# Kernel optimization log

Hardware: AMD Instinct MI355X
Metric: run time of the kernel (lower is better)

## Reference

```python
import jax, jax.numpy as jnp
import numpy as np

H = 128; D_T = 512; D_C = 256
NT = 20000; NC = 100000
E_TC = 100000; E_SIM = 800000; E_TS = 640000
K_APPNP = 10; ALPHA = 0.2


def setup_inputs() -> dict:
    key = jax.random.key(0)
    ki = iter(jax.random.split(key, 64))
    def nrm(shape, scale=1.0):
        return jax.random.normal(next(ki), shape, jnp.float32) * scale
    inp = {
        'table_x': nrm((NT, D_T)),
        'column_x': nrm((NC, D_C)),
        'q': nrm((D_T,)),
    }
    # layer-1 SAGEConv params per edge type: (src_dim, dst_dim)
    dims1 = {'tc': (D_T, D_C), 'rev': (D_C, D_T), 'cs': (D_C, D_C),
             'ns': (D_C, D_C), 'ds': (D_C, D_C), 'ts': (D_T, D_T)}
    for et, (dsrc, ddst) in dims1.items():
        inp['Wl1_' + et] = nrm((dsrc, H), 1.0 / np.sqrt(dsrc))
        inp['bl1_' + et] = jnp.zeros((H,), jnp.float32)
        inp['Wr1_' + et] = nrm((ddst, H), 1.0 / np.sqrt(ddst))
    # layer-2: only the convs that feed the 'table' output are needed
    for et in ('rev', 'ts'):
        inp['Wl2_' + et] = nrm((H, H), 1.0 / np.sqrt(H))
        inp['bl2_' + et] = jnp.zeros((H,), jnp.float32)
        inp['Wr2_' + et] = nrm((H, H), 1.0 / np.sqrt(H))
    inp['Wq'] = nrm((D_T, H), 1.0 / np.sqrt(D_T))
    inp['bq'] = jnp.zeros((H,), jnp.float32)
    inp['Wlin'] = nrm((H, 1), 1.0 / np.sqrt(H))
    inp['blin'] = jnp.zeros((1,), jnp.float32)
    inp['ts_ew'] = jax.random.uniform(next(ki), (E_TS,), jnp.float32)
    inp['tc_src'] = jax.random.randint(next(ki), (E_TC,), 0, NT)
    inp['tc_dst'] = jax.random.randint(next(ki), (E_TC,), 0, NC)
    inp['cs_ei'] = jax.random.randint(next(ki), (2, E_SIM), 0, NC)
    inp['ns_ei'] = jax.random.randint(next(ki), (2, E_SIM), 0, NC)
    inp['ds_ei'] = jax.random.randint(next(ki), (2, E_SIM), 0, NC)
    inp['ts_ei'] = jax.random.randint(next(ki), (2, E_TS), 0, NT)
    return inp


def _sage(xs, xd, src, dst, Wl, bl, Wr, n_dst):
    # PyG SAGEConv: lin_l(mean_{j in N(i)} x_j) + lin_r(x_i).
    # Linear commutes with mean, so project src features first (cheap gather).
    m = (xs @ Wl)[src]                                     # [E, H]
    s = jax.ops.segment_sum(m, dst, num_segments=n_dst)    # [n_dst, H]
    c = jax.ops.segment_sum(jnp.ones(src.shape, m.dtype), dst, num_segments=n_dst)
    return s / jnp.maximum(c, 1.0)[:, None] + bl + xd @ Wr


def _appnp(x, src, dst, ew, n):
    # gcn_norm with self-loops (fill value 1), then K personalized-PageRank steps
    loop = jnp.arange(n)
    s2 = jnp.concatenate([src, loop])
    d2 = jnp.concatenate([dst, loop])
    w2 = jnp.concatenate([ew, jnp.ones((n,), x.dtype)])
    deg = jax.ops.segment_sum(w2, d2, num_segments=n)
    dis = jnp.where(deg > 0, 1.0 / jnp.sqrt(deg), 0.0)
    norm = dis[s2] * w2 * dis[d2]                           # [E+n]
    def step(z, _):
        h = jax.ops.segment_sum(norm[:, None] * z[s2], d2, num_segments=n)
        return (1.0 - ALPHA) * h + ALPHA * x, None
    z, _ = jax.lax.scan(step, x, None, length=K_APPNP)
    return z


def reference(table_x, column_x, q, Wl1_tc, bl1_tc, Wr1_tc, Wl1_rev, bl1_rev, Wr1_rev,
              Wl1_cs, bl1_cs, Wr1_cs, Wl1_ns, bl1_ns, Wr1_ns, Wl1_ds, bl1_ds, Wr1_ds,
              Wl1_ts, bl1_ts, Wr1_ts, Wl2_rev, bl2_rev, Wr2_rev, Wl2_ts, bl2_ts, Wr2_ts,
              Wq, bq, Wlin, blin, ts_ew, tc_src, tc_dst, cs_ei, ns_ei, ds_ei, ts_ei):
    nT, nC = table_x.shape[0], column_x.shape[0]
    # ---- HeteroConv layer 1 (sum over edge types per destination type) ----
    col1 = (_sage(table_x, column_x, tc_src, tc_dst, Wl1_tc, bl1_tc, Wr1_tc, nC)
            + _sage(column_x, column_x, cs_ei[0], cs_ei[1], Wl1_cs, bl1_cs, Wr1_cs, nC)
            + _sage(column_x, column_x, ns_ei[0], ns_ei[1], Wl1_ns, bl1_ns, Wr1_ns, nC)
            + _sage(column_x, column_x, ds_ei[0], ds_ei[1], Wl1_ds, bl1_ds, Wr1_ds, nC))
    tab1 = (_sage(column_x, table_x, tc_dst, tc_src, Wl1_rev, bl1_rev, Wr1_rev, nT)
            + _sage(table_x, table_x, ts_ei[0], ts_ei[1], Wl1_ts, bl1_ts, Wr1_ts, nT))
    col1 = jax.nn.relu(col1)
    tab1 = jax.nn.relu(tab1)
    # ---- HeteroConv layer 2 (only the 'table' output is consumed) ----
    tab2 = (_sage(col1, tab1, tc_dst, tc_src, Wl2_rev, bl2_rev, Wr2_rev, nT)
            + _sage(tab1, tab1, ts_ei[0], ts_ei[1], Wl2_ts, bl2_ts, Wr2_ts, nT))
    # ---- retrieval-weighted query injection ----
    qv = q @ Wq + bq                                        # [H]
    eps = 1e-12
    xr = table_x / jnp.maximum(jnp.linalg.norm(table_x, axis=1, keepdims=True), eps)
    qr = q / jnp.maximum(jnp.linalg.norm(q), eps)
    wgt = jnp.maximum(xr @ qr, 0.0)                         # [nT]
    z0 = wgt[:, None] * qv[None, :]                         # [nT, H]
    # ---- APPNP diffusion over the table-sim graph ----
    z = _appnp(tab2 + z0, ts_ei[0], ts_ei[1], ts_ew, nT)
    return (z @ Wlin + blin)[:, 0]
```

## Files before the change

kernel.cpp:

```cpp
#include <hip/hip_runtime.h>

#define NT 20000
#define NC 100000
#define DT 512
#define DC 256
#define E_TC 100000
#define E_SIM 800000
#define E_TS 640000

#define KB_COL 0
#define KB_TAB (4 * NC)
#define NKEY   (4 * NC + 2 * NT)
#define NED_AB (3 * E_SIM + E_TC + E_TC + E_TS)
#define COLSTR 112
#define TABSTR 96
#define GCOL 782
#define GTAB 313
#define NFILL 365
#define GRID_MEGA (GCOL + GTAB + NFILL)

typedef float f32x4 __attribute__((ext_vector_type(4)));
typedef __bf16 bf16x8 __attribute__((ext_vector_type(8)));


struct WD { const float* w0; const float* w1; const float* w2; const float* w3;
            __bf16* out; int K; int kshift; int ebase; };
struct WD8 { WD d[8]; };

__global__ void wprep_all(WD8 ds, int total) {
    int i = blockIdx.x * blockDim.x + threadIdx.x;
    if (i >= total) return;
#pragma unroll
    for (int s = 7; s >= 0; --s) {
        if (i >= ds.d[s].ebase) {
            const WD d = ds.d[s];
            const int idx = i - d.ebase;
            const int n = idx >> d.kshift;
            const int k = idx & (d.K - 1);
            float v = d.w0[(size_t)k * 128 + n];
            if (d.w1) v += d.w1[(size_t)k * 128 + n];
            if (d.w2) v += d.w2[(size_t)k * 128 + n];
            if (d.w3) v += d.w3[(size_t)k * 128 + n];
            d.out[(size_t)n * d.K + k] = (__bf16)v;
            return;
        }
    }
}

__global__ void vecprep(const float* __restrict__ q, const float* __restrict__ Wq,
                        const float* __restrict__ bq,
                        const float* __restrict__ Wr2_rev, const float* __restrict__ Wr2_ts,
                        const float* __restrict__ Wl2_rev, const float* __restrict__ Wl2_ts,
                        const float* __restrict__ bl2_rev, const float* __restrict__ bl2_ts,
                        const float* __restrict__ Wlin,
                        const float* __restrict__ bl1_tc, const float* __restrict__ bl1_cs,
                        const float* __restrict__ bl1_ns, const float* __restrict__ bl1_ds,
                        const float* __restrict__ bl1_rev, const float* __restrict__ bl1_ts,
                        float* __restrict__ biasC, float* __restrict__ biasT1,
                        float* __restrict__ w2s, float* __restrict__ wrev,
                        float* __restrict__ wts, float* __restrict__ sc) {
    const int t = threadIdx.x;
    biasC[t] = bl1_tc[t] + bl1_cs[t] + bl1_ns[t] + bl1_ds[t];
    biasT1[t] = bl1_rev[t] + bl1_ts[t];
    float a = 0.f, b = 0.f, c = 0.f;
    for (int h = 0; h < 128; ++h) {
        const float wl = Wlin[h];
        a = fmaf(Wr2_rev[(size_t)t * 128 + h] + Wr2_ts[(size_t)t * 128 + h], wl, a);
        b = fmaf(Wl2_rev[(size_t)t * 128 + h], wl, b);
        c = fmaf(Wl2_ts[(size_t)t * 128 + h], wl, c);
    }
    w2s[t] = a; wrev[t] = b; wts[t] = c;
    float qv = bq[t];
    for (int k = 0; k < 512; ++k) qv = fmaf(q[k], Wq[(size_t)k * 128 + t], qv);
    __shared__ float sh[128];
    sh[t] = qv * Wlin[t];
    __syncthreads();
    for (int st = 64; st >= 1; st >>= 1) { if (t < st) sh[t] += sh[t + st]; __syncthreads(); }
    if (t == 0) sc[0] = sh[0];
    __syncthreads();
    sh[t] = (bl2_rev[t] + bl2_ts[t]) * Wlin[t];
    __syncthreads();
    for (int st = 64; st >= 1; st >>= 1) { if (t < st) sh[t] += sh[t + st]; __syncthreads(); }
    if (t == 0) sc[1] = sh[0];
    __syncthreads();
    float ss = 0.f;
    for (int k = t; k < 512; k += 128) { const float v = q[k]; ss = fmaf(v, v, ss); }
    sh[t] = ss;
    __syncthreads();
    for (int st = 64; st >= 1; st >>= 1) { if (t < st) sh[t] += sh[t + st]; __syncthreads(); }
    if (t == 0) sc[2] = fmaxf(sqrtf(sh[0]), 1e-12f);
}


struct B5 { const __bf16* p[5]; };
struct Y5 { __bf16* p[5]; };
struct B3 { const __bf16* p[3]; };
struct Y3 { __bf16* p[3]; };
struct ED { const int* dst; const int* src; int E; int ebase; int ng; int g;
            int keybase; int srcoff; int ts; };
struct ED6 { ED d[6]; };

__launch_bounds__(256, 2)
__global__ void mega(const float* __restrict__ Xc, B5 wpc, const float* __restrict__ biasC,
                     Y5 ypc, const float* __restrict__ Xt, B3 wpt,
                     const float* __restrict__ biasT, Y3 ypt,
                     const float* __restrict__ q, const float* __restrict__ sc,
                     float* __restrict__ wgt, ED6 cds, const float* __restrict__ ew_ts,
                     float* __restrict__ deg, int* __restrict__ cur,
                     int* __restrict__ ed_idx, int2* __restrict__ edT) {
    __shared__ __bf16 Bs[128 * 256];
    const int bb = blockIdx.x;
    const int bt = bb & 3;
    const int t = threadIdx.x;

    if (bt == 3) {
        for (int e = (bb >> 2) * 256 + t; e < NED_AB; e += NFILL * 256) {
#pragma unroll
            for (int i = 5; i >= 0; --i) {
                if (e >= cds.d[i].ebase) {
                    const ED d = cds.d[i];
                    const int le = e - d.ebase;
                    const int dstv = d.dst[le];
                    const int key = d.keybase + dstv * d.ng + d.g;
                    const int srcv = d.src[le];
                    const int slot = atomicAdd(&cur[key], 1);
                    if (key < KB_TAB) {
                        const int g = key & 3;
                        const int cap = (g < 3) ? 32 : 16;
                        if (slot < cap)
                            ed_idx[(key >> 2) * COLSTR + g * 32 + slot] = d.srcoff + srcv;
                    } else {
                        const int k2 = key - KB_TAB;
                        if (k2 & 1) {
                            const float ew = ew_ts[le];
                            atomicAdd(&deg[dstv], ew);
                            if (slot < 72)
                                edT[(k2 >> 1) * TABSTR + 24 + slot] =
                                    make_int2(NC + srcv, __float_as_int(ew));
                        } else {
                            if (slot < 24)
                                edT[(k2 >> 1) * TABSTR + slot] = make_int2(srcv, 0);
                        }
                    }
                    break;
                }
            }
        }
        return;
    }

    const int gi = (bb >> 2) * 3 + bt;
    const int lane = t & 63;
    const int wave = t >> 6;
    const int l15 = lane & 15;
    const int kg = lane >> 4;

    if (gi < GCOL) {
        const int rowbase = gi * 128 + wave * 32;
        bf16x8 af[2][8];
#pragma unroll
        for (int m = 0; m < 2; ++m) {
            int r = rowbase + m * 16 + l15;
            r = (r < NC) ? r : (NC - 1);
            const float* baseA = Xc + (size_t)r * 256 + kg * 8;
#pragma unroll
            for (int ks = 0; ks < 8; ++ks) {
                const float4 x0 = *reinterpret_cast<const float4*>(baseA + ks * 32);
                const float4 x1 = *reinterpret_cast<const float4*>(baseA + ks * 32 + 4);
                bf16x8 tt;
                tt[0] = (__bf16)x0.x; tt[1] = (__bf16)x0.y; tt[2] = (__bf16)x0.z; tt[3] = (__bf16)x0.w;
                tt[4] = (__bf16)x1.x; tt[5] = (__bf16)x1.y; tt[6] = (__bf16)x1.z; tt[7] = (__bf16)x1.w;
                af[m][ks] = tt;
            }
        }
#pragma unroll
        for (int o = 0; o < 5; ++o) {
            __syncthreads();
            const __bf16* Wt = wpc.p[o];
#pragma unroll
            for (int i = 0; i < 16; ++i) {
                const int u = t + i * 256;
                const int row = u >> 5;
                const int ku = u & 31;
                const bf16x8 v = *reinterpret_cast<const bf16x8*>(Wt + (size_t)row * 256 + ku * 8);
                *reinterpret_cast<bf16x8*>(&Bs[row * 256 + ((ku ^ (row & 7)) << 3)]) = v;
            }
            __syncthreads();
            f32x4 acc[2][8];
#pragma unroll
            for (int m = 0; m < 2; ++m)
#pragma unroll
                for (int n = 0; n < 8; ++n) acc[m][n] = (f32x4)0.f;
#pragma unroll
            for (int ks = 0; ks < 8; ++ks) {
                const int ku = ks * 4 + kg;
#pragma unroll
                for (int n = 0; n < 8; ++n) {
                    const int r = n * 16 + l15;
                    const bf16x8 bf = *reinterpret_cast<const bf16x8*>(&Bs[r * 256 + ((ku ^ (r & 7)) << 3)]);
                    acc[0][n] = __builtin_amdgcn_mfma_f32_16x16x32_bf16(af[0][ks], bf, acc[0][n], 0, 0, 0);
                    acc[1][n] = __builtin_amdgcn_mfma_f32_16x16x32_bf16(af[1][ks], bf, acc[1][n], 0, 0, 0);
                }
            }
            __bf16* Y = ypc.p[o];
#pragma unroll
            for (int n = 0; n < 8; ++n) {
                const int col = n * 16 + l15;
                const float bv = (o == 0) ? biasC[col] : 0.f;
#pragma unroll
                for (int m = 0; m < 2; ++m)
#pragma unroll
                    for (int rr = 0; rr < 4; ++rr) {
                        const int row = rowbase + m * 16 + kg * 4 + rr;
                        if (row < NC) Y[(size_t)row * 128 + col] = (__bf16)(acc[m][n][rr] + bv);
                    }
            }
        }
        return;
    }

    {
        const int gb = gi - GCOL;
        const int rowbase = gb * 64 + wave * 16;
        const int r0 = rowbase + l15;
        const bool rv = r0 < NT;
        const int rc = rv ? r0 : (NT - 1);
        const float* baseA = Xt + (size_t)rc * 512 + kg * 8;

        bf16x8 af[16];
        float dot = 0.f, ss = 0.f;
#pragma unroll
        for (int ks = 0; ks < 16; ++ks) {
            const float4 x0 = *reinterpret_cast<const float4*>(baseA + ks * 32);
            const float4 x1 = *reinterpret_cast<const float4*>(baseA + ks * 32 + 4);
            const float4 q0 = *reinterpret_cast<const float4*>(q + kg * 8 + ks * 32);
            const float4 q1 = *reinterpret_cast<const float4*>(q + kg * 8 + ks * 32 + 4);
            dot += x0.x * q0.x + x0.y * q0.y + x0.z * q0.z + x0.w * q0.w
                 + x1.x * q1.x + x1.y * q1.y + x1.z * q1.z + x1.w * q1.w;
            ss += x0.x * x0.x + x0.y * x0.y + x0.z * x0.z + x0.w * x0.w
                + x1.x * x1.x + x1.y * x1.y + x1.z * x1.z + x1.w * x1.w;
            bf16x8 tt;
            tt[0] = (__bf16)x0.x; tt[1] = (__bf16)x0.y; tt[2] = (__bf16)x0.z; tt[3] = (__bf16)x0.w;
            tt[4] = (__bf16)x1.x; tt[5] = (__bf16)x1.y; tt[6] = (__bf16)x1.z; tt[7] = (__bf16)x1.w;
            af[ks] = tt;
        }
        dot += __shfl_xor(dot, 16); dot += __shfl_xor(dot, 32);
        ss  += __shfl_xor(ss, 16);  ss  += __shfl_xor(ss, 32);
        if (lane < 16 && rv) {
            const float nx = fmaxf(sqrtf(ss), 1e-12f);
            wgt[r0] = fmaxf(dot, 0.f) / (nx * sc[2]);
        }
#pragma unroll
        for (int o = 0; o < 3; ++o) {
            f32x4 acc[8];
#pragma unroll
            for (int n = 0; n < 8; ++n) acc[n] = (f32x4)0.f;
            const __bf16* Wt = wpt.p[o];
#pragma unroll
            for (int c = 0; c < 2; ++c) {
                __syncthreads();
#pragma unroll
                for (int i = 0; i < 16; ++i) {
                    const int u = t + i * 256;
                    const int row = u >> 5;
                    const int ku = u & 31;
                    const bf16x8 v = *reinterpret_cast<const bf16x8*>(Wt + (size_t)row * 512 + c * 256 + ku * 8);
                    *reinterpret_cast<bf16x8*>(&Bs[row * 256 + ((ku ^ (row & 7)) << 3)]) = v;
                }
                __syncthreads();
#pragma unroll
                for (int ks = 0; ks < 8; ++ks) {
                    const int ku = ks * 4 + kg;
#pragma unroll
                    for (int n = 0; n < 8; ++n) {
                        const int r = n * 16 + l15;
                        const bf16x8 bf = *reinterpret_cast<const bf16x8*>(&Bs[r * 256 + ((ku ^ (r & 7)) << 3)]);
                        acc[n] = __builtin_amdgcn_mfma_f32_16x16x32_bf16(af[c * 8 + ks], bf, acc[n], 0, 0, 0);
                    }
                }
            }
            __bf16* Y = ypt.p[o];
#pragma unroll
            for (int n = 0; n < 8; ++n) {
                const int col = n * 16 + l15;
                const float bv = (o == 0) ? biasT[col] : 0.f;
#pragma unroll
                for (int rr = 0; rr < 4; ++rr) {
                    const int row = rowbase + kg * 4 + rr;
                    if (row < NT) Y[(size_t)row * 128 + col] = (__bf16)(acc[n][rr] + bv);
                }
            }
        }
    }
}


__global__ void deg_to_dis(float* __restrict__ deg, int n) {
    int i = blockIdx.x * blockDim.x + threadIdx.x;
    if (i < n) {
        float d = deg[i];
        deg[i] = (d > 0.f) ? (1.0f / sqrtf(d)) : 0.f;
    }
}

__global__ void fill_f32(float* __restrict__ p, float v, int n) {
    int i = blockIdx.x * blockDim.x + threadIdx.x;
    if (i < n) p[i] = v;
}

__global__ void nrm_pass(int2* __restrict__ edT, const int* __restrict__ cur,
                         const float* __restrict__ dis) {
    int i = blockIdx.x * blockDim.x + threadIdx.x;
    if (i >= NT * 72) return;
    const int row = i / 72;
    const int s = i - row * 72;
    int lg = cur[KB_TAB + row * 2 + 1];
    lg = (lg < 72) ? lg : 72;
    if (s >= lg) return;
    const int2 v = edT[row * TABSTR + 24 + s];
    const float nv = dis[v.x - NC] * __int_as_float(v.y) * dis[row];
    edT[row * TABSTR + 24 + s].y = __float_as_int(nv);
}


__launch_bounds__(256)
__global__ void col_fused(const __bf16* __restrict__ selfRow, const __bf16* __restrict__ featCat,
                          const int* __restrict__ cur, const int* __restrict__ ed_idx,
                          const float* __restrict__ wvec, float* __restrict__ outv, int n) {
    const int wave = threadIdx.x >> 6;
    const int lane = threadIdx.x & 63;
    const int sg = lane >> 4;
    const int sl = lane & 15;
    const int row = blockIdx.x * 4 + wave;
    if (row >= n) return;
    const int4 l4 = *reinterpret_cast<const int4*>(&cur[row * 4]);
    int len[4];
    len[0] = (l4.x < 32) ? l4.x : 32;
    len[1] = (l4.y < 32) ? l4.y : 32;
    len[2] = (l4.z < 32) ? l4.z : 32;
    len[3] = (l4.w < 16) ? l4.w : 16;
    const int rowbase = row * COLSTR;
    float s8[8] = {0.f, 0.f, 0.f, 0.f, 0.f, 0.f, 0.f, 0.f};
#pragma unroll
    for (int g = 0; g < 4; ++g) {
        const int lg = len[g];
        if (lg <= 0) continue;
        const int base = rowbase + g * 32;
        const float w = 1.0f / (float)lg;
        int j = sg;
        for (; j + 4 < lg; j += 8) {
            const int s0 = ed_idx[base + j];
            const int s1 = ed_idx[base + j + 4];
            const bf16x8 v0 = *reinterpret_cast<const bf16x8*>(&featCat[(size_t)s0 * 128 + sl * 8]);
            const bf16x8 v1 = *reinterpret_cast<const bf16x8*>(&featCat[(size_t)s1 * 128 + sl * 8]);
#pragma unroll
            for (int t = 0; t < 8; ++t) {
                s8[t] = fmaf(w, (float)v0[t], s8[t]);
                s8[t] = fmaf(w, (float)v1[t], s8[t]);
            }
        }
        if (j < lg) {
            const int s0 = ed_idx[base + j];
            const bf16x8 v0 = *reinterpret_cast<const bf16x8*>(&featCat[(size_t)s0 * 128 + sl * 8]);
#pragma unroll
            for (int t = 0; t < 8; ++t) s8[t] = fmaf(w, (float)v0[t], s8[t]);
        }
    }
#pragma unroll
    for (int t = 0; t < 8; ++t) {
        s8[t] += __shfl_xor(s8[t], 16);
        s8[t] += __shfl_xor(s8[t], 32);
    }
    const bf16x8 gv = *reinterpret_cast<const bf16x8*>(&selfRow[(size_t)row * 128 + sl * 8]);
    const float4 w0 = *reinterpret_cast<const float4*>(&wvec[sl * 8]);
    const float4 w1 = *reinterpret_cast<const float4*>(&wvec[sl * 8 + 4]);
    const float ww[8] = {w0.x, w0.y, w0.z, w0.w, w1.x, w1.y, w1.z, w1.w};
    float d = 0.f;
#pragma unroll
    for (int t = 0; t < 8; ++t) d = fmaf(fmaxf(s8[t] + (float)gv[t], 0.f), ww[t], d);
#pragma unroll
    for (int off = 8; off; off >>= 1) d += __shfl_xor(d, off);
    if (lane == 0) outv[row] = d;
}

__launch_bounds__(256)
__global__ void tab_fused(const __bf16* __restrict__ selfRow, const __bf16* __restrict__ featCat,
                          const int* __restrict__ cur, const int2* __restrict__ edT,
                          const float* __restrict__ wa, const float* __restrict__ wb,
                          float* __restrict__ ya, float* __restrict__ yb, int n) {
    const int wave = threadIdx.x >> 6;
    const int lane = threadIdx.x & 63;
    const int sg = lane >> 4;
    const int sl = lane & 15;
    const int row = blockIdx.x * 4 + wave;
    if (row >= n) return;
    const int2 l2 = *reinterpret_cast<const int2*>(&cur[KB_TAB + row * 2]);
    int len[2];
    len[0] = (l2.x < 24) ? l2.x : 24;
    len[1] = (l2.y < 72) ? l2.y : 72;
    const int rowbase = row * TABSTR;
    float s8[8] = {0.f, 0.f, 0.f, 0.f, 0.f, 0.f, 0.f, 0.f};
#pragma unroll
    for (int g = 0; g < 2; ++g) {
        const int lg = len[g];
        if (lg <= 0) continue;
        const int base = rowbase + g * 24;
        const float w = 1.0f / (float)lg;
        int j = sg;
        for (; j + 4 < lg; j += 8) {
            const int s0 = edT[base + j].x;
            const int s1 = edT[base + j + 4].x;
            const bf16x8 v0 = *reinterpret_cast<const bf16x8*>(&featCat[(size_t)s0 * 128 + sl * 8]);
            const bf16x8 v1 = *reinterpret_cast<const bf16x8*>(&featCat[(size_t)s1 * 128 + sl * 8]);
#pragma unroll
            for (int t = 0; t < 8; ++t) {
                s8[t] = fmaf(w, (float)v0[t], s8[t]);
                s8[t] = fmaf(w, (float)v1[t], s8[t]);
            }
        }
        if (j < lg) {
            const int s0 = edT[base + j].x;
            const bf16x8 v0 = *reinterpret_cast<const bf16x8*>(&featCat[(size_t)s0 * 128 + sl * 8]);
#pragma unroll
            for (int t = 0; t < 8; ++t) s8[t] = fmaf(w, (float)v0[t], s8[t]);
        }
    }
#pragma unroll
    for (int t = 0; t < 8; ++t) {
        s8[t] += __shfl_xor(s8[t], 16);
        s8[t] += __shfl_xor(s8[t], 32);
    }
    const bf16x8 gv = *reinterpret_cast<const bf16x8*>(&selfRow[(size_t)row * 128 + sl * 8]);
    const float4 a0 = *reinterpret_cast<const float4*>(&wa[sl * 8]);
    const float4 a1 = *reinterpret_cast<const float4*>(&wa[sl * 8 + 4]);
    const float4 b0 = *reinterpret_cast<const float4*>(&wb[sl * 8]);
    const float4 b1 = *reinterpret_cast<const float4*>(&wb[sl * 8 + 4]);
    const float wwa[8] = {a0.x, a0.y, a0.z, a0.w, a1.x, a1.y, a1.z, a1.w};
    const float wwb[8] = {b0.x, b0.y, b0.z, b0.w, b1.x, b1.y, b1.z, b1.w};
    float da = 0.f, db = 0.f;
#pragma unroll
    for (int t = 0; t < 8; ++t) {
        const float rv = fmaxf(s8[t] + (float)gv[t], 0.f);
        da = fmaf(rv, wwa[t], da);
        db = fmaf(rv, wwb[t], db);
    }
#pragma unroll
    for (int off = 8; off; off >>= 1) { da += __shfl_xor(da, off); db += __shfl_xor(db, off); }
    if (lane == 0) { ya[row] = da; yb[row] = db; }
}


__launch_bounds__(256)
__global__ void y0_joint(const float* __restrict__ tvs, const float* __restrict__ val2,
                         const int* __restrict__ cur, const int2* __restrict__ edT,
                         const float* __restrict__ wgt, const float* __restrict__ sc,
                         float* __restrict__ y0, int n) {
    const int row = blockIdx.x * 16 + (threadIdx.x >> 4);
    const int l = threadIdx.x & 15;
    if (row >= n) return;
    const int2 l2 = *reinterpret_cast<const int2*>(&cur[KB_TAB + row * 2]);
    int len[2];
    len[0] = (l2.x < 24) ? l2.x : 24;
    len[1] = (l2.y < 72) ? l2.y : 72;
    const int rowbase = row * TABSTR;
    float s = 0.f;
#pragma unroll
    for (int g = 0; g < 2; ++g) {
        const int lg = len[g];
        if (lg <= 0) continue;
        const int base = rowbase + g * 24;
        const float w = 1.0f / (float)lg;
        for (int j = l; j < lg; j += 16) {
            int idx = edT[base + j].x;
            if (g == 1) idx -= NC;
            s = fmaf(w, val2[g == 1 ? (NC + idx) : idx], s);
        }
    }
#pragma unroll
    for (int off = 8; off; off >>= 1) s += __shfl_xor(s, off);
    if (l == 0) y0[row] = tvs[row] + sc[1] + wgt[row] * sc[0] + s;
}

__launch_bounds__(256)
__global__ void appnp_s(const float* __restrict__ z, const float* __restrict__ y0,
                        const int* __restrict__ cur, const int2* __restrict__ edT,
                        const float* __restrict__ dis, float* __restrict__ zo,
                        const float* __restrict__ blin, float* __restrict__ out,
                        int n, int last) {
    const int row = blockIdx.x * 16 + (threadIdx.x >> 4);
    const int l = threadIdx.x & 15;
    if (row >= n) return;
    int lg = cur[KB_TAB + row * 2 + 1];
    lg = (lg < 72) ? lg : 72;
    const int base = row * TABSTR + 24;
    float s = 0.f;
    int j = l;
    for (; j + 16 < lg; j += 32) {
        const int2 p0 = edT[base + j];
        const int2 p1 = edT[base + j + 16];
        s = fmaf(__int_as_float(p0.y), z[p0.x - NC], s);
        s = fmaf(__int_as_float(p1.y), z[p1.x - NC], s);
    }
    if (j < lg) {
        const int2 p0 = edT[base + j];
        s = fmaf(__int_as_float(p0.y), z[p0.x - NC], s);
    }
#pragma unroll
    for (int off = 8; off; off >>= 1) s += __shfl_xor(s, off);
    if (l == 0) {
        const float d = dis[row];
        const float v = 0.8f * (s + d * d * z[row]) + 0.2f * y0[row];
        if (last) out[row] = v + blin[0];
        else zo[row] = v;
    }
}


extern "C" void kernel_launch(void* const* d_in, const int* in_sizes, int n_in,
                              void* d_out, int out_size, void* d_ws, size_t ws_size,
                              hipStream_t stream) {
    const float* table_x  = (const float*)d_in[0];
    const float* column_x = (const float*)d_in[1];
    const float* q        = (const float*)d_in[2];
    const float* Wl1_tc  = (const float*)d_in[3];  const float* bl1_tc  = (const float*)d_in[4];  const float* Wr1_tc  = (const float*)d_in[5];
    const float* Wl1_rev = (const float*)d_in[6];  const float* bl1_rev = (const float*)d_in[7];  const float* Wr1_rev = (const float*)d_in[8];
    const float* Wl1_cs  = (const float*)d_in[9];  const float* bl1_cs  = (const float*)d_in[10]; const float* Wr1_cs  = (const float*)d_in[11];
    const float* Wl1_ns  = (const float*)d_in[12]; const float* bl1_ns  = (const float*)d_in[13]; const float* Wr1_ns  = (const float*)d_in[14];
    const float* Wl1_ds  = (const float*)d_in[15]; const float* bl1_ds  = (const float*)d_in[16]; const float* Wr1_ds  = (const float*)d_in[17];
    const float* Wl1_ts  = (const float*)d_in[18]; const float* bl1_ts  = (const float*)d_in[19]; const float* Wr1_ts  = (const float*)d_in[20];
    const float* Wl2_rev = (const float*)d_in[21]; const float* bl2_rev = (const float*)d_in[22]; const float* Wr2_rev = (const float*)d_in[23];
    const float* Wl2_ts  = (const float*)d_in[24]; const float* bl2_ts  = (const float*)d_in[25]; const float* Wr2_ts  = (const float*)d_in[26];
    const float* Wq   = (const float*)d_in[27]; const float* bq   = (const float*)d_in[28];
    const float* Wlin = (const float*)d_in[29]; const float* blin = (const float*)d_in[30];
    const float* ts_ew = (const float*)d_in[31];
    const int* tc_src = (const int*)d_in[32];
    const int* tc_dst = (const int*)d_in[33];
    const int* cs_ei  = (const int*)d_in[34];
    const int* ns_ei  = (const int*)d_in[35];
    const int* ds_ei  = (const int*)d_in[36];
    const int* ts_ei  = (const int*)d_in[37];

    char* w = (char*)d_ws;
    size_t off = 0;
    auto alloc = [&](size_t bytes) -> void* {
        void* p = w + off;
        off += (bytes + 255) & ~(size_t)255;
        return p;
    };
    __bf16* featC = (__bf16*)alloc(((size_t)3 * NC + NT) * 128 * 2);
    __bf16* featT = (__bf16*)alloc(((size_t)NC + NT) * 128 * 2);
    __bf16* projC_cs  = featC;
    __bf16* projC_ns  = featC + (size_t)NC * 128;
    __bf16* projC_ds  = featC + (size_t)2 * NC * 128;
    __bf16* projT_tc  = featC + (size_t)3 * NC * 128;
    __bf16* projC_rev = featT;
    __bf16* projT_ts  = featT + (size_t)NC * 128;
    __bf16* gemmC = (__bf16*)alloc((size_t)NC * 128 * 2);
    __bf16* gemmT = (__bf16*)alloc((size_t)NT * 128 * 2);
    float* val2  = (float*)alloc((size_t)(NC + NT) * 4);
    float* f_colv = val2;
    float* f_tvt  = val2 + NC;
    float* f_tvs = (float*)alloc((size_t)NT * 4);
    float* f_wgt = (float*)alloc((size_t)NT * 4);
    float* f_dis = (float*)alloc((size_t)NT * 4);
    float* f_y0  = (float*)alloc((size_t)NT * 4);
    float* f_za  = (float*)alloc((size_t)NT * 4);
    float* f_zb  = (float*)alloc((size_t)NT * 4);
    __bf16* WtS1c  = (__bf16*)alloc((size_t)128 * 256 * 2);
    __bf16* Wt_cs  = (__bf16*)alloc((size_t)128 * 256 * 2);
    __bf16* Wt_ns  = (__bf16*)alloc((size_t)128 * 256 * 2);
    __bf16* Wt_ds  = (__bf16*)alloc((size_t)128 * 256 * 2);
    __bf16* Wt_rev = (__bf16*)alloc((size_t)128 * 256 * 2);
    __bf16* Wt_tc  = (__bf16*)alloc((size_t)128 * 512 * 2);
    __bf16* WtS1t  = (__bf16*)alloc((size_t)128 * 512 * 2);
    __bf16* Wt_ts  = (__bf16*)alloc((size_t)128 * 512 * 2);
    float* f_biasC  = (float*)alloc(128 * 4);
    float* f_biasT1 = (float*)alloc(128 * 4);
    float* f_w2s  = (float*)alloc(128 * 4);
    float* f_wrev = (float*)alloc(128 * 4);
    float* f_wts  = (float*)alloc(128 * 4);
    float* f_sc   = (float*)alloc(16 * 4);
    int* i_cur  = (int*)alloc((size_t)NKEY * 4);
    int* ed_idx = (int*)alloc((size_t)NC * COLSTR * 4);
    int2* edT   = (int2*)alloc((size_t)NT * TABSTR * 8);
    if (off > ws_size) return;

    auto cdiv = [](int a, int b) { return (a + b - 1) / b; };

    {
        WD8 ds;
        int eb = 0;
        auto set = [&](int i, const float* a, const float* b2, const float* c, const float* d2,
                       __bf16* o, int K, int ksh) {
            ds.d[i] = {a, b2, c, d2, o, K, ksh, eb};
            eb += 128 * K;
        };
        set(0, Wr1_tc, Wr1_cs, Wr1_ns, Wr1_ds, WtS1c, 256, 8);
        set(1, Wl1_cs, nullptr, nullptr, nullptr, Wt_cs, 256, 8);
        set(2, Wl1_ns, nullptr, nullptr, nullptr, Wt_ns, 256, 8);
        set(3, Wl1_ds, nullptr, nullptr, nullptr, Wt_ds, 256, 8);
        set(4, Wl1_rev, nullptr, nullptr, nullptr, Wt_rev, 256, 8);
        set(5, Wl1_tc, nullptr, nullptr, nullptr, Wt_tc, 512, 9);
        set(6, Wr1_rev, Wr1_ts, nullptr, nullptr, WtS1t, 512, 9);
        set(7, Wl1_ts, nullptr, nullptr, nullptr, Wt_ts, 512, 9);
        wprep_all<<<cdiv(eb, 256), 256, 0, stream>>>(ds, eb);
    }
    vecprep<<<1, 128, 0, stream>>>(q, Wq, bq, Wr2_rev, Wr2_ts, Wl2_rev, Wl2_ts,
                                   bl2_rev, bl2_ts, Wlin, bl1_tc, bl1_cs, bl1_ns, bl1_ds,
                                   bl1_rev, bl1_ts, f_biasC, f_biasT1,
                                   f_w2s, f_wrev, f_wts, f_sc);

    fill_f32<<<cdiv(NT, 256), 256, 0, stream>>>(f_dis, 1.0f, NT);
    hipMemsetAsync(i_cur, 0, (size_t)NKEY * 4, stream);

    ED6 cds;
    cds.d[0] = {cs_ei + E_SIM, cs_ei, E_SIM, 0,                  4, 0, KB_COL, 0,      0};
    cds.d[1] = {ns_ei + E_SIM, ns_ei, E_SIM, E_SIM,              4, 1, KB_COL, NC,     0};
    cds.d[2] = {ds_ei + E_SIM, ds_ei, E_SIM, 2 * E_SIM,          4, 2, KB_COL, 2 * NC, 0};
    cds.d[3] = {tc_dst, tc_src, E_TC, 3 * E_SIM,                 4, 3, KB_COL, 3 * NC, 0};
    cds.d[4] = {tc_src, tc_dst, E_TC, 3 * E_SIM + E_TC,          2, 0, KB_TAB, 0,      0};
    cds.d[5] = {ts_ei + E_TS, ts_ei, E_TS, 3 * E_SIM + 2 * E_TC, 2, 1, KB_TAB, NC,     1};

    {
        B5 wpc; wpc.p[0] = WtS1c; wpc.p[1] = Wt_cs; wpc.p[2] = Wt_ns; wpc.p[3] = Wt_ds; wpc.p[4] = Wt_rev;
        Y5 ypc; ypc.p[0] = gemmC; ypc.p[1] = projC_cs; ypc.p[2] = projC_ns; ypc.p[3] = projC_ds; ypc.p[4] = projC_rev;
        B3 wpt; wpt.p[0] = WtS1t; wpt.p[1] = Wt_tc; wpt.p[2] = Wt_ts;
        Y3 ypt; ypt.p[0] = gemmT; ypt.p[1] = projT_tc; ypt.p[2] = projT_ts;
        mega<<<GRID_MEGA, 256, 0, stream>>>(column_x, wpc, f_biasC, ypc,
                                            table_x, wpt, f_biasT1, ypt,
                                            q, f_sc, f_wgt, cds, ts_ew,
                                            f_dis, i_cur, ed_idx, edT);
    }

    deg_to_dis<<<cdiv(NT, 256), 256, 0, stream>>>(f_dis, NT);
    nrm_pass<<<cdiv(NT * 72, 256), 256, 0, stream>>>(edT, i_cur, f_dis);

    col_fused<<<cdiv(NC, 4), 256, 0, stream>>>(gemmC, featC, i_cur, ed_idx,
                                               f_wrev, f_colv, NC);
    tab_fused<<<cdiv(NT, 4), 256, 0, stream>>>(gemmT, featT, i_cur, edT,
                                               f_w2s, f_wts, f_tvs, f_tvt, NT);

    y0_joint<<<cdiv(NT, 16), 256, 0, stream>>>(f_tvs, val2, i_cur, edT,
                                               f_wgt, f_sc, f_y0, NT);

    const float* zin = f_y0;
    float* zout = f_za;
    for (int it = 0; it < 10; ++it) {
        const int last = (it == 9);
        appnp_s<<<cdiv(NT, 16), 256, 0, stream>>>(zin, f_y0, i_cur, edT,
                                                  f_dis, zout, blin, (float*)d_out, NT, last);
        zin = zout;
        zout = (zout == f_za) ? f_zb : f_za;
    }
}
```

Measured before the change: 579.5 us.

## Fold edge-bucket fill into extra waves inside each GEMM block of mega kernel

Drops the separate fill-only blocks from the fused projection/edge-bucketing kernel. Each GEMM block now gets two extra waves (384 threads) that do the atomic edge bucketing in chunks between the GEMM barriers, so the fill work runs alongside the MFMA work inside the same workgroup. It also simplifies the index arithmetic in y0_joint's gather. The intent is better overlap of latency-bound atomics with compute, at the cost of higher register and occupancy pressure from launch_bounds(384,3) and fill progress being tied to the GEMM barrier cadence.

```diff
diff --git a/kernel.cpp b/kernel.cpp
--- a/kernel.cpp
+++ b/kernel.cpp
@@ -16,8 +16,8 @@
 #define TABSTR 96
 #define GCOL 782
 #define GTAB 313
-#define NFILL 365
-#define GRID_MEGA (GCOL + GTAB + NFILL)
+#define GRID_MEGA (GCOL + GTAB)
+#define FILL_LANES (GRID_MEGA * 128)
 
 typedef float f32x4 __attribute__((ext_vector_type(4)));
 typedef __bf16 bf16x8 __attribute__((ext_vector_type(8)));
@@ -100,127 +100,141 @@
             int keybase; int srcoff; int ts; };
 struct ED6 { ED d[6]; };
 
-__launch_bounds__(256, 2)
-__global__ void mega(const float* __restrict__ Xc, B5 wpc, const float* __restrict__ biasC,
-                     Y5 ypc, const float* __restrict__ Xt, B3 wpt,
-                     const float* __restrict__ biasT, Y3 ypt,
-                     const float* __restrict__ q, const float* __restrict__ sc,
-                     float* __restrict__ wgt, ED6 cds, const float* __restrict__ ew_ts,
-                     float* __restrict__ deg, int* __restrict__ cur,
-                     int* __restrict__ ed_idx, int2* __restrict__ edT) {
+__launch_bounds__(384, 3)
+__global__ void mega2(const float* __restrict__ Xc, B5 wpc, const float* __restrict__ biasC,
+                      Y5 ypc, const float* __restrict__ Xt, B3 wpt,
+                      const float* __restrict__ biasT, Y3 ypt,
+                      const float* __restrict__ q, const float* __restrict__ sc,
+                      float* __restrict__ wgt, ED6 cds, const float* __restrict__ ew_ts,
+                      float* __restrict__ deg, int* __restrict__ cur,
+                      int* __restrict__ ed_idx, int2* __restrict__ edT) {
     __shared__ __bf16 Bs[128 * 256];
     const int bb = blockIdx.x;
-    const int bt = bb & 3;
     const int t = threadIdx.x;
-
-    if (bt == 3) {
-        for (int e = (bb >> 2) * 256 + t; e < NED_AB; e += NFILL * 256) {
-#pragma unroll
-            for (int i = 5; i >= 0; --i) {
-                if (e >= cds.d[i].ebase) {
-                    const ED d = cds.d[i];
-                    const int le = e - d.ebase;
-                    const int dstv = d.dst[le];
-                    const int key = d.keybase + dstv * d.ng + d.g;
-                    const int srcv = d.src[le];
-                    const int slot = atomicAdd(&cur[key], 1);
-                    if (key < KB_TAB) {
-                        const int g = key & 3;
-                        const int cap = (g < 3) ? 32 : 16;
-                        if (slot < cap)
-                            ed_idx[(key >> 2) * COLSTR + g * 32 + slot] = d.srcoff + srcv;
+    const bool fillw = (t >= 256);
+    int fe = bb * 128 + (t - 256);
+
+    auto fill_edge = [&](int e) {
+#pragma unroll
+        for (int i = 5; i >= 0; --i) {
+            if (e >= cds.d[i].ebase) {
+                const ED d = cds.d[i];
+                const int le = e - d.ebase;
+                const int dstv = d.dst[le];
+                const int key = d.keybase + dstv * d.ng + d.g;
+                const int srcv = d.src[le];
+                const int slot = atomicAdd(&cur[key], 1);
+                if (key < KB_TAB) {
+                    const int g = key & 3;
+                    const int cap = (g < 3) ? 32 : 16;
+                    if (slot < cap)
+                        ed_idx[(key >> 2) * COLSTR + g * 32 + slot] = d.srcoff + srcv;
+                } else {
+                    const int k2 = key - KB_TAB;
+                    if (k2 & 1) {
+                        const float ew = ew_ts[le];
+                        atomicAdd(&deg[dstv], ew);
+                        if (slot < 72)
+                            edT[(k2 >> 1) * TABSTR + 24 + slot] =
+                                make_int2(NC + srcv, __float_as_int(ew));
                     } else {
-                        const int k2 = key - KB_TAB;
-                        if (k2 & 1) {
-                            const float ew = ew_ts[le];
-                            atomicAdd(&deg[dstv], ew);
-                            if (slot < 72)
-                                edT[(k2 >> 1) * TABSTR + 24 + slot] =
-                                    make_int2(NC + srcv, __float_as_int(ew));
-                        } else {
-                            if (slot < 24)
-                                edT[(k2 >> 1) * TABSTR + slot] = make_int2(srcv, 0);
-                        }
+                        if (slot < 24)
+                            edT[(k2 >> 1) * TABSTR + slot] = make_int2(srcv, 0);
                     }
-                    break;
-                }
-            }
-        }
-        return;
-    }
-
-    const int gi = (bb >> 2) * 3 + bt;
+                }
+                return;
+            }
+        }
+    };
+    auto fill_chunk = [&](int n) {
+        for (int it = 0; it < n && fe < NED_AB; ++it) {
+            fill_edge(fe);
+            fe += FILL_LANES;
+        }
+    };
+
     const int lane = t & 63;
     const int wave = t >> 6;
     const int l15 = lane & 15;
     const int kg = lane >> 4;
 
-    if (gi < GCOL) {
-        const int rowbase = gi * 128 + wave * 32;
+    if (bb < GCOL) {
+        const int rowbase = bb * 128 + wave * 32;
         bf16x8 af[2][8];
-#pragma unroll
-        for (int m = 0; m < 2; ++m) {
-            int r = rowbase + m * 16 + l15;
-            r = (r < NC) ? r : (NC - 1);
-            const float* baseA = Xc + (size_t)r * 256 + kg * 8;
-#pragma unroll
-            for (int ks = 0; ks < 8; ++ks) {
-                const float4 x0 = *reinterpret_cast<const float4*>(baseA + ks * 32);
-                const float4 x1 = *reinterpret_cast<const float4*>(baseA + ks * 32 + 4);
-                bf16x8 tt;
-                tt[0] = (__bf16)x0.x; tt[1] = (__bf16)x0.y; tt[2] = (__bf16)x0.z; tt[3] = (__bf16)x0.w;
-                tt[4] = (__bf16)x1.x; tt[5] = (__bf16)x1.y; tt[6] = (__bf16)x1.z; tt[7] = (__bf16)x1.w;
-                af[m][ks] = tt;
+        if (!fillw) {
+#pragma unroll
+            for (int m = 0; m < 2; ++m) {
+                int r = rowbase + m * 16 + l15;
+                r = (r < NC) ? r : (NC - 1);
+                const float* baseA = Xc + (size_t)r * 256 + kg * 8;
+#pragma unroll
+                for (int ks = 0; ks < 8; ++ks) {
+                    const float4 x0 = *reinterpret_cast<const float4*>(baseA + ks * 32);
+                    const float4 x1 = *reinterpret_cast<const float4*>(baseA + ks * 32 + 4);
+                    bf16x8 tt;
+                    tt[0] = (__bf16)x0.x; tt[1] = (__bf16)x0.y; tt[2] = (__bf16)x0.z; tt[3] = (__bf16)x0.w;
+                    tt[4] = (__bf16)x1.x; tt[5] = (__bf16)x1.y; tt[6] = (__bf16)x1.z; tt[7] = (__bf16)x1.w;
+                    af[m][ks] = tt;
+                }
             }
         }
 #pragma unroll
         for (int o = 0; o < 5; ++o) {
             __syncthreads();
-            const __bf16* Wt = wpc.p[o];
-#pragma unroll
-            for (int i = 0; i < 16; ++i) {
-                const int u = t + i * 256;
-                const int row = u >> 5;
-                const int ku = u & 31;
-                const bf16x8 v = *reinterpret_cast<const bf16x8*>(Wt + (size_t)row * 256 + ku * 8);
-                *reinterpret_cast<bf16x8*>(&Bs[row * 256 + ((ku ^ (row & 7)) << 3)]) = v;
+            if (!fillw) {
+                const __bf16* Wt = wpc.p[o];
+#pragma unroll
+                for (int i = 0; i < 16; ++i) {
+                    const int u = t + i * 256;
+                    const int row = u >> 5;
+                    const int ku = u & 31;
+                    const bf16x8 v = *reinterpret_cast<const bf16x8*>(Wt + (size_t)row * 256 + ku * 8);
+                    *reinterpret_cast<bf16x8*>(&Bs[row * 256 + ((ku ^ (row & 7)) << 3)]) = v;
+                }
             }
             __syncthreads();
-            f32x4 acc[2][8];
-#pragma unroll
-            for (int m = 0; m < 2; ++m)
-#pragma unroll
-                for (int n = 0; n < 8; ++n) acc[m][n] = (f32x4)0.f;
-#pragma unroll
-            for (int ks = 0; ks < 8; ++ks) {
-                const int ku = ks * 4 + kg;
+            if (!fillw) {
+                f32x4 acc[2][8];
+#pragma unroll
+                for (int m = 0; m < 2; ++m)
+#pragma unroll
+                    for (int n = 0; n < 8; ++n) acc[m][n] = (f32x4)0.f;
+#pragma unroll
+                for (int ks = 0; ks < 8; ++ks) {
+                    const int ku = ks * 4 + kg;
+#pragma unroll
+                    for (int n = 0; n < 8; ++n) {
+                        const int r = n * 16 + l15;
+                        const bf16x8 bf = *reinterpret_cast<const bf16x8*>(&Bs[r * 256 + ((ku ^ (r & 7)) << 3)]);
+                        acc[0][n] = __builtin_amdgcn_mfma_f32_16x16x32_bf16(af[0][ks], bf, acc[0][n], 0, 0, 0);
+                        acc[1][n] = __builtin_amdgcn_mfma_f32_16x16x32_bf16(af[1][ks], bf, acc[1][n], 0, 0, 0);
+                    }
+                }
+                __bf16* Y = ypc.p[o];
 #pragma unroll
                 for (int n = 0; n < 8; ++n) {
-                    const int r = n * 16 + l15;
-                    const bf16x8 bf = *reinterpret_cast<const bf16x8*>(&Bs[r * 256 + ((ku ^ (r & 7)) << 3)]);
-                    acc[0][n] = __builtin_amdgcn_mfma_f32_16x16x32_bf16(af[0][ks], bf, acc[0][n], 0, 0, 0);
-                    acc[1][n] = __builtin_amdgcn_mfma_f32_16x16x32_bf16(af[1][ks], bf, acc[1][n], 0, 0, 0);
-                }
-            }
-            __bf16* Y = ypc.p[o];
-#pragma unroll
-            for (int n = 0; n < 8; ++n) {
-                const int col = n * 16 + l15;
-                const float bv = (o == 0) ? biasC[col] : 0.f;
-#pragma unroll
-                for (int m = 0; m < 2; ++m)
-#pragma unroll
-                    for (int rr = 0; rr < 4; ++rr) {
-                        const int row = rowbase + m * 16 + kg * 4 + rr;
-                        if (row < NC) Y[(size_t)row * 128 + col] = (__bf16)(acc[m][n][rr] + bv);
-                    }
-            }
+                    const int col = n * 16 + l15;
+                    const float bv = (o == 0) ? biasC[col] : 0.f;
+#pragma unroll
+                    for (int m = 0; m < 2; ++m)
+#pragma unroll
+                        for (int rr = 0; rr < 4; ++rr) {
+                            const int row = rowbase + m * 16 + kg * 4 + rr;
+                            if (row < NC) Y[(size_t)row * 128 + col] = (__bf16)(acc[m][n][rr] + bv);
+                        }
+                }
+            } else {
+                fill_chunk(5);
+            }
+        }
+        if (fillw) {
+            while (fe < NED_AB) { fill_edge(fe); fe += FILL_LANES; }
         }
         return;
     }
 
     {
-        const int gb = gi - GCOL;
+        const int gb = bb - GCOL;
         const int rowbase = gb * 64 + wave * 16;
         const int r0 = rowbase + l15;
         const bool rv = r0 < NT;
@@ -228,27 +242,29 @@
         const float* baseA = Xt + (size_t)rc * 512 + kg * 8;
 
         bf16x8 af[16];
-        float dot = 0.f, ss = 0.f;
-#pragma unroll
-        for (int ks = 0; ks < 16; ++ks) {
-            const float4 x0 = *reinterpret_cast<const float4*>(baseA + ks * 32);
-            const float4 x1 = *reinterpret_cast<const float4*>(baseA + ks * 32 + 4);
-            const float4 q0 = *reinterpret_cast<const float4*>(q + kg * 8 + ks * 32);
-            const float4 q1 = *reinterpret_cast<const float4*>(q + kg * 8 + ks * 32 + 4);
-            dot += x0.x * q0.x + x0.y * q0.y + x0.z * q0.z + x0.w * q0.w
-                 + x1.x * q1.x + x1.y * q1.y + x1.z * q1.z + x1.w * q1.w;
-            ss += x0.x * x0.x + x0.y * x0.y + x0.z * x0.z + x0.w * x0.w
-                + x1.x * x1.x + x1.y * x1.y + x1.z * x1.z + x1.w * x1.w;
-            bf16x8 tt;
-            tt[0] = (__bf16)x0.x; tt[1] = (__bf16)x0.y; tt[2] = (__bf16)x0.z; tt[3] = (__bf16)x0.w;
-            tt[4] = (__bf16)x1.x; tt[5] = (__bf16)x1.y; tt[6] = (__bf16)x1.z; tt[7] = (__bf16)x1.w;
-            af[ks] = tt;
-        }
-        dot += __shfl_xor(dot, 16); dot += __shfl_xor(dot, 32);
-        ss  += __shfl_xor(ss, 16);  ss  += __shfl_xor(ss, 32);
-        if (lane < 16 && rv) {
-            const float nx = fmaxf(sqrtf(ss), 1e-12f);
-            wgt[r0] = fmaxf(dot, 0.f) / (nx * sc[2]);
+        if (!fillw) {
+            float dot = 0.f, ss = 0.f;
+#pragma unroll
+            for (int ks = 0; ks < 16; ++ks) {
+                const float4 x0 = *reinterpret_cast<const float4*>(baseA + ks * 32);
+                const float4 x1 = *reinterpret_cast<const float4*>(baseA + ks * 32 + 4);
+                const float4 q0 = *reinterpret_cast<const float4*>(q + kg * 8 + ks * 32);
+                const float4 q1 = *reinterpret_cast<const float4*>(q + kg * 8 + ks * 32 + 4);
+                dot += x0.x * q0.x + x0.y * q0.y + x0.z * q0.z + x0.w * q0.w
+                     + x1.x * q1.x + x1.y * q1.y + x1.z * q1.z + x1.w * q1.w;
+                ss += x0.x * x0.x + x0.y * x0.y + x0.z * x0.z + x0.w * x0.w
+                    + x1.x * x1.x + x1.y * x1.y + x1.z * x1.z + x1.w * x1.w;
+                bf16x8 tt;
+                tt[0] = (__bf16)x0.x; tt[1] = (__bf16)x0.y; tt[2] = (__bf16)x0.z; tt[3] = (__bf16)x0.w;
+                tt[4] = (__bf16)x1.x; tt[5] = (__bf16)x1.y; tt[6] = (__bf16)x1.z; tt[7] = (__bf16)x1.w;
+                af[ks] = tt;
+            }
+            dot += __shfl_xor(dot, 16); dot += __shfl_xor(dot, 32);
+            ss  += __shfl_xor(ss, 16);  ss  += __shfl_xor(ss, 32);
+            if (lane < 16 && rv) {
+                const float nx = fmaxf(sqrtf(ss), 1e-12f);
+                wgt[r0] = fmaxf(dot, 0.f) / (nx * sc[2]);
+            }
         }
 #pragma unroll
         for (int o = 0; o < 3; ++o) {
@@ -259,37 +275,48 @@
 #pragma unroll
             for (int c = 0; c < 2; ++c) {
                 __syncthreads();
-#pragma unroll
-                for (int i = 0; i < 16; ++i) {
-                    const int u = t + i * 256;
-                    const int row = u >> 5;
-                    const int ku = u & 31;
-                    const bf16x8 v = *reinterpret_cast<const bf16x8*>(Wt + (size_t)row * 512 + c * 256 + ku * 8);
-                    *reinterpret_cast<bf16x8*>(&Bs[row * 256 + ((ku ^ (row & 7)) << 3)]) = v;
+                if (!fillw) {
+#pragma unroll
+                    for (int i = 0; i < 16; ++i) {
+                        const int u = t + i * 256;
+                        const int row = u >> 5;
+                        const int ku = u & 31;
+                        const bf16x8 v = *reinterpret_cast<const bf16x8*>(Wt + (size_t)row * 512 + c * 256 + ku * 8);
+                        *reinterpret_cast<bf16x8*>(&Bs[row * 256 + ((ku ^ (row & 7)) << 3)]) = v;
+                    }
                 }
                 __syncthreads();
-#pragma unroll
-                for (int ks = 0; ks < 8; ++ks) {
-                    const int ku = ks * 4 + kg;
-#pragma unroll
-                    for (int n = 0; n < 8; ++n) {
-                        const int r = n * 16 + l15;
-                        const bf16x8 bf = *reinterpret_cast<const bf16x8*>(&Bs[r * 256 + ((ku ^ (r & 7)) << 3)]);
-                        acc[n] = __builtin_amdgcn_mfma_f32_16x16x32_bf16(af[c * 8 + ks], bf, acc[n], 0, 0, 0);
+                if (!fillw) {
+#pragma unroll
+                    for (int ks = 0; ks < 8; ++ks) {
+                        const int ku = ks * 4 + kg;
+#pragma unroll
+                        for (int n = 0; n < 8; ++n) {
+                            const int r = n * 16 + l15;
+                            const bf16x8 bf = *reinterpret_cast<const bf16x8*>(&Bs[r * 256 + ((ku ^ (r & 7)) << 3)]);
+                            acc[n] = __builtin_amdgcn_mfma_f32_16x16x32_bf16(af[c * 8 + ks], bf, acc[n], 0, 0, 0);
+                        }
                     }
-                }
-            }
-            __bf16* Y = ypt.p[o];
-#pragma unroll
-            for (int n = 0; n < 8; ++n) {
-                const int col = n * 16 + l15;
-                const float bv = (o == 0) ? biasT[col] : 0.f;
-#pragma unroll
-                for (int rr = 0; rr < 4; ++rr) {
-                    const int row = rowbase + kg * 4 + rr;
-                    if (row < NT) Y[(size_t)row * 128 + col] = (__bf16)(acc[n][rr] + bv);
-                }
-            }
+                } else {
+                    fill_chunk(4);
+                }
+            }
+            if (!fillw) {
+                __bf16* Y = ypt.p[o];
+#pragma unroll
+                for (int n = 0; n < 8; ++n) {
+                    const int col = n * 16 + l15;
+                    const float bv = (o == 0) ? biasT[col] : 0.f;
+#pragma unroll
+                    for (int rr = 0; rr < 4; ++rr) {
+                        const int row = rowbase + kg * 4 + rr;
+                        if (row < NT) Y[(size_t)row * 128 + col] = (__bf16)(acc[n][rr] + bv);
+                    }
+                }
+            }
+        }
+        if (fillw) {
+            while (fe < NED_AB) { fill_edge(fe); fe += FILL_LANES; }
         }
     }
 }
@@ -471,9 +498,8 @@
         const int base = rowbase + g * 24;
         const float w = 1.0f / (float)lg;
         for (int j = l; j < lg; j += 16) {
-            int idx = edT[base + j].x;
-            if (g == 1) idx -= NC;
-            s = fmaf(w, val2[g == 1 ? (NC + idx) : idx], s);
+            const int idx = edT[base + j].x;
+            s = fmaf(w, val2[idx], s);
         }
     }
 #pragma unroll
@@ -626,10 +652,10 @@
         Y5 ypc; ypc.p[0] = gemmC; ypc.p[1] = projC_cs; ypc.p[2] = projC_ns; ypc.p[3] = projC_ds; ypc.p[4] = projC_rev;
         B3 wpt; wpt.p[0] = WtS1t; wpt.p[1] = Wt_tc; wpt.p[2] = Wt_ts;
         Y3 ypt; ypt.p[0] = gemmT; ypt.p[1] = projT_tc; ypt.p[2] = projT_ts;
-        mega<<<GRID_MEGA, 256, 0, stream>>>(column_x, wpc, f_biasC, ypc,
-                                            table_x, wpt, f_biasT1, ypt,
-                                            q, f_sc, f_wgt, cds, ts_ew,
-                                            f_dis, i_cur, ed_idx, edT);
+        mega2<<<GRID_MEGA, 384, 0, stream>>>(column_x, wpc, f_biasC, ypc,
+                                             table_x, wpt, f_biasT1, ypt,
+                                             q, f_sc, f_wgt, cds, ts_ew,
+                                             f_dis, i_cur, ed_idx, edT);
     }
 
     deg_to_dis<<<cdiv(NT, 256), 256, 0, stream>>>(f_dis, NT);
```

Result: slower. 601.6 us (+3.8%).
